# Performance work log

Hardware: AMD Instinct MI355X
Metric: run time of the kernel (lower is better)

The kernel has to match this reference:

```python
import jax, jax.numpy as jnp
import numpy as np

E = 131072   # total messages
N = 8192     # dim_size (num nodes)
D = 256      # input_dim == hidden_dim (forced by h + m add)


def setup_inputs() -> dict:
    key = jax.random.key(0)
    k1, k2, k3, k4, k5 = jax.random.split(key, 5)
    msg = jax.random.normal(k1, (E, D), dtype=jnp.float32)
    index = jax.random.randint(k2, (E,), 0, N)
    t = jax.random.uniform(k3, (E,), dtype=jnp.float32)
    # torch.nn.Linear(D, D) params (kaiming-uniform-ish scale)
    W = jax.random.normal(k4, (D, D), dtype=jnp.float32) / np.sqrt(D)
    b = (jax.random.normal(k5, (D,), dtype=jnp.float32) * 0.01)
    return {"msg": msg, "index": index, "t": t, "dim_size": N, "W": W, "b": b}


def reference(msg, index, t, dim_size, W, b):
    # Original: for each node, sort its messages by t, then run the linear
    # recurrence h <- W @ (m + h) + b starting from h = 0; nodes with no
    # messages keep h = 0. Vectorized: one global stable sort by (index, t),
    # then a single segmented lax.scan with reset at segment boundaries.
    num_msgs, d = msg.shape
    order = jnp.lexsort((t, index))          # primary key: index, secondary: t
    m_sorted = msg[order]                     # [E, d]
    seg = index[order]                        # [E]

    def step(carry, inp):
        h, prev = carry
        m, s = inp
        h_in = jnp.where(s == prev, h, jnp.zeros_like(h))  # reset at new segment
        h_new = (m + h_in) @ W.T + b
        return (h_new, s), h_new

    init = (jnp.zeros((d,), msg.dtype), jnp.asarray(-1, seg.dtype))
    _, ys = jax.lax.scan(step, init, (m_sorted, seg))      # ys: [E, d]

    # final hidden per node = h at the last message of its segment
    pos = jnp.arange(num_msgs)
    last = jax.ops.segment_max(pos, seg, num_segments=dim_size)
    counts = jax.ops.segment_sum(jnp.ones((num_msgs,), jnp.int32), seg,
                                 num_segments=dim_size)
    gathered = ys[jnp.clip(last, 0, num_msgs - 1)]          # [N, d]
    hidden = jnp.where((counts > 0)[:, None], gathered, jnp.zeros_like(gathered))
    return hidden
```

## Files before the change

### kernel.cpp

```cpp
#include <hip/hip_runtime.h>
#include <hip/hip_bf16.h>

#define E_MSGS 131072
#define N_NODES 8192
#define D_DIM 256
#define XA_STRIDE 264

typedef __bf16 bf16x8 __attribute__((ext_vector_type(8)));
typedef float f32x4 __attribute__((ext_vector_type(4)));

#define BAR() asm volatile("s_waitcnt lgkmcnt(0)\n\ts_barrier" ::: "memory")


__global__ void k_count(const int* __restrict__ index, int* __restrict__ counts) {
    int e = blockIdx.x * blockDim.x + threadIdx.x;
    if (e < E_MSGS) atomicAdd(&counts[index[e]], 1);
}

__global__ void k_prep(const int* __restrict__ counts, int* __restrict__ offsets,
                       int* __restrict__ perm) {
    __shared__ int partial[256];
    __shared__ int hist[256];
    __shared__ int hscan[256];
    __shared__ int hcur[256];
    int tid = threadIdx.x;
    hist[tid] = 0;
    __syncthreads();

    int base = tid * 32;
    int local[32];
    int sum = 0;
#pragma unroll
    for (int i = 0; i < 32; i++) {
        local[i] = sum;
        int c = counts[base + i];
        sum += c;
        atomicAdd(&hist[min(c, 255)], 1);
    }
    partial[tid] = sum;
    __syncthreads();
    for (int off = 1; off < 256; off <<= 1) {
        int v = (tid >= off) ? partial[tid - off] : 0;
        __syncthreads();
        partial[tid] += v;
        __syncthreads();
    }
    int basesum = (tid > 0) ? partial[tid - 1] : 0;
#pragma unroll
    for (int i = 0; i < 32; i++) offsets[base + i] = basesum + local[i];
    if (tid == 255) offsets[N_NODES] = partial[255];

    hscan[tid] = hist[255 - tid];
    __syncthreads();
    for (int off = 1; off < 256; off <<= 1) {
        int v = (tid >= off) ? hscan[tid - off] : 0;
        __syncthreads();
        hscan[tid] += v;
        __syncthreads();
    }
    hcur[tid] = hscan[255 - tid] - hist[tid];
    __syncthreads();
#pragma unroll
    for (int i = 0; i < 32; i++) {
        int n = base + i;
        int c = min(counts[n], 255);
        int pos = atomicAdd(&hcur[c], 1);
        perm[pos] = n;
    }
}

__global__ void k_scatter(const int* __restrict__ index, const int* __restrict__ offsets,
                          int* __restrict__ cursors, int* __restrict__ bucket) {
    int e = blockIdx.x * blockDim.x + threadIdx.x;
    if (e < E_MSGS) {
        int n = index[e];
        int p = offsets[n] + atomicAdd(&cursors[n], 1);
        bucket[p] = e;
    }
}

__global__ void k_sortseg(const float* __restrict__ t, const int* __restrict__ offsets,
                          const int* __restrict__ bucket, int* __restrict__ sorted_id) {
    int wid = (blockIdx.x * 256 + threadIdx.x) >> 6;
    int ln = threadIdx.x & 63;
    int beg = offsets[wid], end = offsets[wid + 1];
    int cnt = end - beg;
    int e = 0; float tv = 0.f;
    if (ln < cnt) { e = bucket[beg + ln]; tv = t[e]; }
    int rank = 0;
    for (int j = 0; j < cnt; j++) {
        float tj = __shfl(tv, j);
        int ej = __shfl(e, j);
        rank += (tj < tv) || (tj == tv && ej < e);
    }
    if (ln < cnt) sorted_id[beg + rank] = e;
}


__launch_bounds__(256, 2)
__global__ void k_gru(const float* __restrict__ msg, const float* __restrict__ W,
                      const float* __restrict__ b, const int* __restrict__ offsets,
                      const int* __restrict__ sorted_id, const int* __restrict__ perm,
                      float* __restrict__ out) {
    __shared__ __bf16 xA[2][16 * XA_STRIDE];

    int tid  = threadIdx.x;
    int wave = tid >> 6;
    int lane = tid & 63;
    int q    = lane >> 4;
    int l    = lane & 15;
    int node0 = blockIdx.x * 16;

    bf16x8 wf[8][4];
#pragma unroll
    for (int t4 = 0; t4 < 4; t4++) {
        const float* wr = W + (64 * wave + 16 * t4 + l) * D_DIM;
#pragma unroll
        for (int c = 0; c < 8; c++) {
            int k0 = 32 * c + 8 * q;
            float4 w0 = *(const float4*)(wr + k0);
            float4 w1 = *(const float4*)(wr + k0 + 4);
            bf16x8 f;
            f[0] = (__bf16)w0.x; f[1] = (__bf16)w0.y; f[2] = (__bf16)w0.z; f[3] = (__bf16)w0.w;
            f[4] = (__bf16)w1.x; f[5] = (__bf16)w1.y; f[6] = (__bf16)w1.z; f[7] = (__bf16)w1.w;
            wf[c][t4] = f;
        }
    }
    float bias[4];
#pragma unroll
    for (int t4 = 0; t4 < 4; t4++) bias[t4] = b[64 * wave + 16 * t4 + l];

    int nodeC[4], off4[4], cnt4[4];
#pragma unroll
    for (int r = 0; r < 4; r++) {
        int n = perm[node0 + 4 * q + r];
        nodeC[r] = n;
        off4[r] = offsets[n];
        cnt4[r] = offsets[n + 1] - off4[r];
    }
    int nfirst = perm[node0];
    int S = offsets[nfirst + 1] - offsets[nfirst];

    float h[4][4];
#pragma unroll
    for (int t4 = 0; t4 < 4; t4++)
#pragma unroll
        for (int r = 0; r < 4; r++) h[t4][r] = 0.f;

    float mvA[4][4], mvB[4][4];
    int sidp[4];
#pragma unroll
    for (int r = 0; r < 4; r++) {
        int sid0 = sorted_id[min(off4[r], E_MSGS - 1)];
        int sid1 = sorted_id[min(off4[r] + 1, E_MSGS - 1)];
        const float* m0 = msg + (long)sid0 * D_DIM;
        const float* m1 = msg + (long)sid1 * D_DIM;
#pragma unroll
        for (int t4 = 0; t4 < 4; t4++) {
            int col = 64 * wave + 16 * t4 + l;
            xA[0][(4 * q + r) * XA_STRIDE + col] = (__bf16)m0[col];
            mvA[r][t4] = m1[col];
        }
        sidp[r] = sorted_id[min(off4[r] + 2, E_MSGS - 1)];
    }
    BAR();

    auto step = [&](int s, float (&cur)[4][4], float (&nxt)[4][4]) {
#pragma unroll
        for (int r = 0; r < 4; r++) {
            const float* mrow = msg + (long)sidp[r] * D_DIM;
#pragma unroll
            for (int t4 = 0; t4 < 4; t4++) nxt[r][t4] = mrow[64 * wave + 16 * t4 + l];
        }
#pragma unroll
        for (int r = 0; r < 4; r++)
            sidp[r] = sorted_id[min(off4[r] + s + 3, E_MSGS - 1)];

        const __bf16* buf = xA[s & 1];
        f32x4 acc[4];
#pragma unroll
        for (int t4 = 0; t4 < 4; t4++) acc[t4] = (f32x4){0.f, 0.f, 0.f, 0.f};
#pragma unroll
        for (int c = 0; c < 8; c++) {
            bf16x8 a = *(const bf16x8*)(buf + l * XA_STRIDE + 32 * c + 8 * q);
#pragma unroll
            for (int t4 = 0; t4 < 4; t4++)
                acc[t4] = __builtin_amdgcn_mfma_f32_16x16x32_bf16(a, wf[c][t4], acc[t4], 0, 0, 0);
        }

        __bf16* nbuf = xA[(s + 1) & 1];
#pragma unroll
        for (int t4 = 0; t4 < 4; t4++) {
#pragma unroll
            for (int r = 0; r < 4; r++) {
                float hn = acc[t4][r] + bias[t4];
                bool valid = s < cnt4[r];
                h[t4][r] = valid ? hn : h[t4][r];
                nbuf[(4 * q + r) * XA_STRIDE + 64 * wave + 16 * t4 + l] =
                    (__bf16)(h[t4][r] + cur[r][t4]);
            }
        }
        BAR();
    };

    int s = 0;
    while (s < S) {
        step(s, mvA, mvB);
        s++;
        if (s >= S) break;
        step(s, mvB, mvA);
        s++;
    }

#pragma unroll
    for (int t4 = 0; t4 < 4; t4++)
#pragma unroll
        for (int r = 0; r < 4; r++)
            out[(long)nodeC[r] * D_DIM + 64 * wave + 16 * t4 + l] = h[t4][r];
}


extern "C" void kernel_launch(void* const* d_in, const int* in_sizes, int n_in,
                              void* d_out, int out_size, void* d_ws, size_t ws_size,
                              hipStream_t stream) {
    const float* msg   = (const float*)d_in[0];
    const int*   index = (const int*)d_in[1];
    const float* t     = (const float*)d_in[2];
    const float* W     = (const float*)d_in[4];
    const float* b     = (const float*)d_in[5];
    float* out = (float*)d_out;

    int* ws = (int*)d_ws;
    int* counts    = ws;
    int* cursors   = ws + 8192;
    int* offsets   = ws + 16384;
    int* perm      = ws + 24584;
    int* bucket    = ws + 32776;
    int* sorted_id = ws + 163848;

    hipMemsetAsync(counts, 0, 16384 * sizeof(int), stream);

    k_count<<<E_MSGS / 256, 256, 0, stream>>>(index, counts);
    k_prep<<<1, 256, 0, stream>>>(counts, offsets, perm);
    k_scatter<<<E_MSGS / 256, 256, 0, stream>>>(index, offsets, cursors, bucket);
    k_sortseg<<<N_NODES * 64 / 256, 256, 0, stream>>>(t, offsets, bucket, sorted_id);
    k_gru<<<N_NODES / 16, 256, 0, stream>>>(msg, W, b, offsets, sorted_id, perm, out);
}
```

Before: 256.4 us.

## Stage sorted ids in LDS, deepen message prefetch, widen prep kernel

Result: slower. 267.7 us (+4.4%).

```diff
diff --git a/kernel.cpp b/kernel.cpp
--- a/kernel.cpp
+++ b/kernel.cpp
@@ -4,7 +4,8 @@
 #define E_MSGS 131072
 #define N_NODES 8192
 #define D_DIM 256
-#define XA_STRIDE 264
+#define XA_STRIDE 280
+#define SMAX 64
 
 typedef __bf16 bf16x8 __attribute__((ext_vector_type(8)));
 typedef float f32x4 __attribute__((ext_vector_type(4)));
@@ -19,53 +20,54 @@
 
 __global__ void k_prep(const int* __restrict__ counts, int* __restrict__ offsets,
                        int* __restrict__ perm) {
-    __shared__ int partial[256];
+    __shared__ int partial[1024];
     __shared__ int hist[256];
-    __shared__ int hscan[256];
     __shared__ int hcur[256];
     int tid = threadIdx.x;
-    hist[tid] = 0;
-    __syncthreads();
-
-    int base = tid * 32;
-    int local[32];
+    if (tid < 256) hist[tid] = 0;
+    __syncthreads();
+
+    int base = tid * 8;
+    int4 c0 = ((const int4*)counts)[tid * 2];
+    int4 c1 = ((const int4*)counts)[tid * 2 + 1];
+    int cs[8] = {c0.x, c0.y, c0.z, c0.w, c1.x, c1.y, c1.z, c1.w};
+    int local[8];
     int sum = 0;
 #pragma unroll
-    for (int i = 0; i < 32; i++) {
+    for (int i = 0; i < 8; i++) {
         local[i] = sum;
-        int c = counts[base + i];
-        sum += c;
-        atomicAdd(&hist[min(c, 255)], 1);
+        sum += cs[i];
+        atomicAdd(&hist[min(cs[i], 255)], 1);
     }
     partial[tid] = sum;
     __syncthreads();
+    for (int off = 1; off < 1024; off <<= 1) {
+        int v = (tid >= off) ? partial[tid - off] : 0;
+        __syncthreads();
+        partial[tid] += v;
+        __syncthreads();
+    }
+    int basesum = (tid > 0) ? partial[tid - 1] : 0;
+#pragma unroll
+    for (int i = 0; i < 8; i++) offsets[base + i] = basesum + local[i];
+    if (tid == 1023) offsets[N_NODES] = partial[1023];
+    __syncthreads();
+
+    if (tid < 256) partial[tid] = hist[255 - tid];
+    __syncthreads();
     for (int off = 1; off < 256; off <<= 1) {
-        int v = (tid >= off) ? partial[tid - off] : 0;
-        __syncthreads();
-        partial[tid] += v;
-        __syncthreads();
-    }
-    int basesum = (tid > 0) ? partial[tid - 1] : 0;
-#pragma unroll
-    for (int i = 0; i < 32; i++) offsets[base + i] = basesum + local[i];
-    if (tid == 255) offsets[N_NODES] = partial[255];
-
-    hscan[tid] = hist[255 - tid];
-    __syncthreads();
-    for (int off = 1; off < 256; off <<= 1) {
-        int v = (tid >= off) ? hscan[tid - off] : 0;
-        __syncthreads();
-        hscan[tid] += v;
-        __syncthreads();
-    }
-    hcur[tid] = hscan[255 - tid] - hist[tid];
-    __syncthreads();
-#pragma unroll
-    for (int i = 0; i < 32; i++) {
-        int n = base + i;
-        int c = min(counts[n], 255);
+        int v = (tid < 256 && tid >= off) ? partial[tid - off] : 0;
+        __syncthreads();
+        if (tid < 256) partial[tid] += v;
+        __syncthreads();
+    }
+    if (tid < 256) hcur[tid] = partial[255 - tid] - hist[tid];
+    __syncthreads();
+#pragma unroll
+    for (int i = 0; i < 8; i++) {
+        int c = min(cs[i], 255);
         int pos = atomicAdd(&hcur[c], 1);
-        perm[pos] = n;
+        perm[pos] = base + i;
     }
 }
 
@@ -103,6 +105,7 @@
                       const int* __restrict__ sorted_id, const int* __restrict__ perm,
                       float* __restrict__ out) {
     __shared__ __bf16 xA[2][16 * XA_STRIDE];
+    __shared__ int sidT[16][SMAX];
 
     int tid  = threadIdx.x;
     int wave = tid >> 6;
@@ -130,16 +133,26 @@
 #pragma unroll
     for (int t4 = 0; t4 < 4; t4++) bias[t4] = b[64 * wave + 16 * t4 + l];
 
-    int nodeC[4], off4[4], cnt4[4];
+    int nodeC[4], cnt4[4];
 #pragma unroll
     for (int r = 0; r < 4; r++) {
         int n = perm[node0 + 4 * q + r];
         nodeC[r] = n;
-        off4[r] = offsets[n];
-        cnt4[r] = offsets[n + 1] - off4[r];
+        cnt4[r] = offsets[n + 1] - offsets[n];
     }
     int nfirst = perm[node0];
-    int S = offsets[nfirst + 1] - offsets[nfirst];
+    int S = min(offsets[nfirst + 1] - offsets[nfirst], SMAX);
+
+    {
+        int i = tid >> 4;
+        int ni = perm[node0 + i];
+        int o0 = offsets[ni];
+        int cn = offsets[ni + 1] - o0;
+#pragma unroll
+        for (int j = tid & 15; j < SMAX; j += 16)
+            sidT[i][j] = (cn > 0) ? sorted_id[o0 + min(j, cn - 1)] : 0;
+    }
+    BAR();
 
     float h[4][4];
 #pragma unroll
@@ -147,34 +160,37 @@
 #pragma unroll
         for (int r = 0; r < 4; r++) h[t4][r] = 0.f;
 
-    float mvA[4][4], mvB[4][4];
-    int sidp[4];
-#pragma unroll
-    for (int r = 0; r < 4; r++) {
-        int sid0 = sorted_id[min(off4[r], E_MSGS - 1)];
-        int sid1 = sorted_id[min(off4[r] + 1, E_MSGS - 1)];
-        const float* m0 = msg + (long)sid0 * D_DIM;
-        const float* m1 = msg + (long)sid1 * D_DIM;
-#pragma unroll
-        for (int t4 = 0; t4 < 4; t4++) {
-            int col = 64 * wave + 16 * t4 + l;
-            xA[0][(4 * q + r) * XA_STRIDE + col] = (__bf16)m0[col];
-            mvA[r][t4] = m1[col];
-        }
-        sidp[r] = sorted_id[min(off4[r] + 2, E_MSGS - 1)];
+    float mvA[4][4], mvB[4][4], mvC[4][4];
+#pragma unroll
+    for (int r = 0; r < 4; r++) {
+        const float* m0 = msg + (long)sidT[4 * q + r][0] * D_DIM;
+#pragma unroll
+        for (int t4 = 0; t4 < 4; t4++)
+            xA[0][(4 * q + r) * XA_STRIDE + 64 * wave + 16 * t4 + l] =
+                (__bf16)m0[64 * wave + 16 * t4 + l];
+    }
+#pragma unroll
+    for (int r = 0; r < 4; r++) {
+        const float* m1 = msg + (long)sidT[4 * q + r][1] * D_DIM;
+#pragma unroll
+        for (int t4 = 0; t4 < 4; t4++) mvA[r][t4] = m1[64 * wave + 16 * t4 + l];
+    }
+#pragma unroll
+    for (int r = 0; r < 4; r++) {
+        const float* m2 = msg + (long)sidT[4 * q + r][2] * D_DIM;
+#pragma unroll
+        for (int t4 = 0; t4 < 4; t4++) mvB[r][t4] = m2[64 * wave + 16 * t4 + l];
     }
     BAR();
 
     auto step = [&](int s, float (&cur)[4][4], float (&nxt)[4][4]) {
+        int slot = min(s + 3, SMAX - 1);
 #pragma unroll
         for (int r = 0; r < 4; r++) {
-            const float* mrow = msg + (long)sidp[r] * D_DIM;
+            const float* mrow = msg + (long)sidT[4 * q + r][slot] * D_DIM;
 #pragma unroll
             for (int t4 = 0; t4 < 4; t4++) nxt[r][t4] = mrow[64 * wave + 16 * t4 + l];
         }
-#pragma unroll
-        for (int r = 0; r < 4; r++)
-            sidp[r] = sorted_id[min(off4[r] + s + 3, E_MSGS - 1)];
 
         const __bf16* buf = xA[s & 1];
         f32x4 acc[4];
@@ -205,11 +221,11 @@
 
     int s = 0;
     while (s < S) {
-        step(s, mvA, mvB);
-        s++;
+        step(s, mvA, mvC); s++;
         if (s >= S) break;
-        step(s, mvB, mvA);
-        s++;
+        step(s, mvB, mvA); s++;
+        if (s >= S) break;
+        step(s, mvC, mvB); s++;
     }
 
 #pragma unroll
@@ -241,7 +257,7 @@
     hipMemsetAsync(counts, 0, 16384 * sizeof(int), stream);
 
     k_count<<<E_MSGS / 256, 256, 0, stream>>>(index, counts);
-    k_prep<<<1, 256, 0, stream>>>(counts, offsets, perm);
+    k_prep<<<1, 1024, 0, stream>>>(counts, offsets, perm);
     k_scatter<<<E_MSGS / 256, 256, 0, stream>>>(index, offsets, cursors, bucket);
     k_sortseg<<<N_NODES * 64 / 256, 256, 0, stream>>>(t, offsets, bucket, sorted_id);
     k_gru<<<N_NODES / 16, 256, 0, stream>>>(msg, W, b, offsets, sorted_id, perm, out);
```
